# Performance work log

Measured on AMD Instinct MI355X. Metric: run time of the kernel, lower is better.

The kernel has to match this reference:

```python
import jax, jax.numpy as jnp
import numpy as np

B, D, C = 32768, 1024, 40  # batch, proj_dim, num_classes('culture')


def setup_inputs() -> dict:
    key = jax.random.key(0)
    k1, k2, k3, k4, k5 = jax.random.split(key, 5)
    scale = 1.0 / np.sqrt(D)
    return {
        "src": jax.random.normal(k1, (B, D), dtype=jnp.float32),
        "attn_mask": jnp.ones((B,), dtype=jnp.float32),  # unpacked but unused by BiChain
        # padded weights: row i uses only first D+i columns; the rest hit zero buffer slots
        "W": jax.random.normal(k2, (C, D + C), dtype=jnp.float32) * scale,
        "b": jax.random.normal(k3, (C,), dtype=jnp.float32) * scale,
        "W_rev": jax.random.normal(k4, (C, D + C), dtype=jnp.float32) * scale,
        "b_rev": jax.random.normal(k5, (C,), dtype=jnp.float32) * scale,
    }


def _chain(src, W, b):
    """Sequential classifier chain: score_i = sigmoid(<[src, s_0..s_{i-1}], w_i> + b_i)."""
    Bsz, Df = src.shape
    Cn = W.shape[0]
    # growing feature buffer, pre-padded with zeros for future scores
    buf0 = jnp.zeros((Bsz, Df + Cn), dtype=src.dtype).at[:, :Df].set(src)

    def step(buf, inp):
        w_i, b_i, i = inp
        score = jax.nn.sigmoid(buf @ w_i + b_i)            # [B]
        buf = jax.lax.dynamic_update_slice(buf, score[:, None], (0, Df + i))
        return buf, score

    _, scores = jax.lax.scan(step, buf0, (W, b, jnp.arange(Cn)))
    return scores.T  # [B, C]


def reference(src, attn_mask, W, b, W_rev, b_rev):
    out_fwd = _chain(src, W, b)
    out_rev = _chain(src, W_rev, b_rev)
    return (out_fwd + out_rev[:, ::-1]) * 0.5
```

## Files before the change

kernel.cpp:

```cpp
#include <hip/hip_runtime.h>
#include <math.h>

using short8  = __attribute__((ext_vector_type(8))) short;
using short4v = __attribute__((ext_vector_type(4))) short;
using float4v = __attribute__((ext_vector_type(4))) float;

#define D_DIM 1024
#define NCLS  40
#define WSTR  1064
#define TM    64
#define KC    64
#define NCHUNK 16
#define APAD  72

__device__ __forceinline__ short f2bf(float f) {
    union { float f; unsigned u; } x; x.f = f;
    unsigned r = (x.u + 0x7fffu + ((x.u >> 16) & 1u)) >> 16;
    return (short)r;
}

__global__ void convert_w_kernel(const float* __restrict__ W, const float* __restrict__ Wr,
                                 short* __restrict__ Wb) {
    int idx = blockIdx.x * 256 + threadIdx.x;
    int c = idx >> 10;
    int k = idx & 1023;
    float v = (c < NCLS) ? W[c * WSTR + k] : Wr[(c - NCLS) * WSTR + k];
    Wb[idx] = f2bf(v);
}

__global__ __launch_bounds__(256, 3) void bichain_main(
    const float* __restrict__ src, const short* __restrict__ Wb,
    const float* __restrict__ Wf, const float* __restrict__ Wr,
    const float* __restrict__ bf_, const float* __restrict__ br_,
    float* __restrict__ out)
{
    __shared__ __align__(16) unsigned char smem[41472];
    short* As = (short*)smem;
    short* Ws = (short*)(smem + 18432);

    const int tid  = threadIdx.x;
    const int lane = tid & 63;
    const int wave = tid >> 6;
    const int row0 = blockIdx.x * TM;

    const int s_row = tid >> 2;
    const int s_c4  = tid & 3;
    const float* srcRow = src + (long)(row0 + s_row) * D_DIM + s_c4 * 4;

    float4v a_reg[4];
    short8  w_reg[3];
    float4v acc[5];
#pragma unroll
    for (int t = 0; t < 5; ++t)
#pragma unroll
        for (int r = 0; r < 4; ++r) acc[t][r] = 0.f;

    auto load_regs = [&](int ch) {
        const int k0 = ch * KC;
#pragma unroll
        for (int j = 0; j < 4; ++j)
            a_reg[j] = *(const float4v*)(srcRow + k0 + j * 16);
#pragma unroll
        for (int r = 0; r < 3; ++r) {
            int idx = r * 256 + tid;
            if (r < 2 || tid < 128) {
                int cls = idx >> 3, oct = idx & 7;
                w_reg[r] = *(const short8*)(Wb + cls * D_DIM + k0 + oct * 8);
            }
        }
    };

    auto write_lds = [&](int buf) {
        short* Ab = As + buf * (TM * APAD);
#pragma unroll
        for (int j = 0; j < 4; ++j) {
            short4v v;
            v.x = f2bf(a_reg[j].x); v.y = f2bf(a_reg[j].y);
            v.z = f2bf(a_reg[j].z); v.w = f2bf(a_reg[j].w);
            *(short4v*)(Ab + s_row * APAD + j * 16 + s_c4 * 4) = v;
        }
        short* Wbuf = Ws + buf * (80 * APAD);
#pragma unroll
        for (int r = 0; r < 3; ++r) {
            int idx = r * 256 + tid;
            if (r < 2 || tid < 128) {
                int cls = idx >> 3, oct = idx & 7;
                *(short8*)(Wbuf + cls * APAD + oct * 8) = w_reg[r];
            }
        }
    };

    const int lrow = lane & 15;
    const int lk8  = (lane >> 4) * 8;

    auto compute = [&](int buf) {
        const short* Ab = As + buf * (TM * APAD) + (wave * 16) * APAD;
        const short* Wp = Ws + buf * (80 * APAD);
#pragma unroll
        for (int ks = 0; ks < 2; ++ks) {
            short8 af = *(const short8*)(Ab + lrow * APAD + ks * 32 + lk8);
#pragma unroll
            for (int t = 0; t < 5; ++t) {
                short8 bfr = *(const short8*)(Wp + (t * 16 + lrow) * APAD + ks * 32 + lk8);
                acc[t] = __builtin_amdgcn_mfma_f32_16x16x32_bf16(af, bfr, acc[t], 0, 0, 0);
            }
        }
    };

    load_regs(0);
    write_lds(0);
    __syncthreads();
#pragma unroll 1
    for (int ch = 0; ch < NCHUNK; ++ch) {
        const int cur = ch & 1;
        if (ch < NCHUNK - 1) load_regs(ch + 1);
        compute(cur);
        if (ch < NCHUNK - 1) {
            write_lds(cur ^ 1);
            __syncthreads();
        }
    }
    __syncthreads();

    float* Lg = (float*)smem;
    float* Sc = (float*)(smem + 20992);
#pragma unroll
    for (int t = 0; t < 5; ++t)
#pragma unroll
        for (int r = 0; r < 4; ++r) {
            int row = wave * 16 + (lane >> 4) * 4 + r;
            int cls = t * 16 + (lane & 15);
            Lg[row * 81 + cls] = acc[t][r];
        }
    __syncthreads();

    if (tid < 128) {
        const int row = tid >> 1;
        const int dir = tid & 1;
        const float* Wt = dir ? Wr : Wf;
        const float* bi = dir ? br_ : bf_;
        float s[NCLS];
#pragma unroll
        for (int i = 0; i < NCLS; ++i) {
            float z = Lg[row * 81 + dir * NCLS + i] + bi[i];
#pragma unroll
            for (int j = 0; j < i; ++j)
                z += s[j] * Wt[i * WSTR + D_DIM + j];
            s[i] = 1.f / (1.f + __expf(-z));
            Sc[row * 80 + dir * NCLS + i] = s[i];
        }
    }
    __syncthreads();

    float* outp = out + (long)row0 * NCLS;
    for (int idx = tid; idx < TM * NCLS; idx += 256) {
        int row = idx / NCLS;
        int c   = idx - row * NCLS;
        outp[idx] = 0.5f * (Sc[row * 80 + c] + Sc[row * 80 + NCLS + (NCLS - 1 - c)]);
    }
}

extern "C" void kernel_launch(void* const* d_in, const int* in_sizes, int n_in,
                              void* d_out, int out_size, void* d_ws, size_t ws_size,
                              hipStream_t stream) {
    const float* src = (const float*)d_in[0];
    const float* W   = (const float*)d_in[2];
    const float* b   = (const float*)d_in[3];
    const float* Wr  = (const float*)d_in[4];
    const float* br  = (const float*)d_in[5];
    float* out = (float*)d_out;
    short* Wb  = (short*)d_ws;

    convert_w_kernel<<<320, 256, 0, stream>>>(W, Wr, Wb);
    bichain_main<<<512, 256, 0, stream>>>(src, Wb, W, Wr, b, br, out);
}
```

Before: 42.15 us.

## Load MFMA operands directly from global memory, removing LDS staging and barriers

The GEMM main loop no longer stages A and W tiles through double-buffered LDS with a __syncthreads per chunk. Each lane now loads its src fragment straight from global memory, prefetched one chunk ahead, converts it to bf16 in registers, and reads W fragments directly from the bf16 weight buffer. This removes LDS write/read traffic and block barriers, at the cost of uncoalesced, strided global reads (each wave reads 16 rows and each lane reads W rows strided by D). The change also lowers the launch-bounds occupancy hint and switches to the library bf16 conversion.

```diff
diff --git a/kernel.cpp b/kernel.cpp
--- a/kernel.cpp
+++ b/kernel.cpp
@@ -1,22 +1,20 @@
 #include <hip/hip_runtime.h>
+#include <hip/hip_bf16.h>
 #include <math.h>
 
 using short8  = __attribute__((ext_vector_type(8))) short;
-using short4v = __attribute__((ext_vector_type(4))) short;
 using float4v = __attribute__((ext_vector_type(4))) float;
 
 #define D_DIM 1024
 #define NCLS  40
 #define WSTR  1064
 #define TM    64
-#define KC    64
 #define NCHUNK 16
-#define APAD  72
 
 __device__ __forceinline__ short f2bf(float f) {
-    union { float f; unsigned u; } x; x.f = f;
-    unsigned r = (x.u + 0x7fffu + ((x.u >> 16) & 1u)) >> 16;
-    return (short)r;
+    __hip_bfloat16 h = __float2bfloat16(f);
+    union { __hip_bfloat16 h; short s; } u; u.h = h;
+    return u.s;
 }
 
 __global__ void convert_w_kernel(const float* __restrict__ W, const float* __restrict__ Wr,
@@ -28,102 +26,65 @@
     Wb[idx] = f2bf(v);
 }
 
-__global__ __launch_bounds__(256, 3) void bichain_main(
+__global__ __launch_bounds__(256, 2) void bichain_main(
     const float* __restrict__ src, const short* __restrict__ Wb,
     const float* __restrict__ Wf, const float* __restrict__ Wr,
     const float* __restrict__ bf_, const float* __restrict__ br_,
     float* __restrict__ out)
 {
-    __shared__ __align__(16) unsigned char smem[41472];
-    short* As = (short*)smem;
-    short* Ws = (short*)(smem + 18432);
+    __shared__ float Lg[TM * 81];
+    __shared__ float Sc[TM * 80];
 
     const int tid  = threadIdx.x;
     const int lane = tid & 63;
     const int wave = tid >> 6;
     const int row0 = blockIdx.x * TM;
+    const int lrow = lane & 15;
+    const int lk8  = (lane >> 4) * 8;
 
-    const int s_row = tid >> 2;
-    const int s_c4  = tid & 3;
-    const float* srcRow = src + (long)(row0 + s_row) * D_DIM + s_c4 * 4;
+    const float* aRow = src + (size_t)(row0 + wave * 16 + lrow) * D_DIM + lk8;
+    const short* wRow = Wb + lrow * D_DIM + lk8;
 
-    float4v a_reg[4];
-    short8  w_reg[3];
     float4v acc[5];
 #pragma unroll
     for (int t = 0; t < 5; ++t)
 #pragma unroll
         for (int r = 0; r < 4; ++r) acc[t][r] = 0.f;
 
-    auto load_regs = [&](int ch) {
-        const int k0 = ch * KC;
+    float4v apre[4];
 #pragma unroll
-        for (int j = 0; j < 4; ++j)
-            a_reg[j] = *(const float4v*)(srcRow + k0 + j * 16);
+    for (int j = 0; j < 4; ++j)
+        apre[j] = *(const float4v*)(aRow + (j >> 1) * 32 + (j & 1) * 4);
+
+#pragma unroll 1
+    for (int ch = 0; ch < NCHUNK; ++ch) {
+        float4v a[4];
 #pragma unroll
-        for (int r = 0; r < 3; ++r) {
-            int idx = r * 256 + tid;
-            if (r < 2 || tid < 128) {
-                int cls = idx >> 3, oct = idx & 7;
-                w_reg[r] = *(const short8*)(Wb + cls * D_DIM + k0 + oct * 8);
+        for (int j = 0; j < 4; ++j) a[j] = apre[j];
+        if (ch < NCHUNK - 1) {
+            const float* nx = aRow + (ch + 1) * 64;
+#pragma unroll
+            for (int j = 0; j < 4; ++j)
+                apre[j] = *(const float4v*)(nx + (j >> 1) * 32 + (j & 1) * 4);
+        }
+        short8 af[2];
+#pragma unroll
+        for (int ks = 0; ks < 2; ++ks)
+#pragma unroll
+            for (int e = 0; e < 4; ++e) {
+                af[ks][e]     = f2bf(a[2 * ks][e]);
+                af[ks][e + 4] = f2bf(a[2 * ks + 1][e]);
             }
-        }
-    };
-
-    auto write_lds = [&](int buf) {
-        short* Ab = As + buf * (TM * APAD);
+        const short* wc = wRow + ch * 64;
 #pragma unroll
-        for (int j = 0; j < 4; ++j) {
-            short4v v;
-            v.x = f2bf(a_reg[j].x); v.y = f2bf(a_reg[j].y);
-            v.z = f2bf(a_reg[j].z); v.w = f2bf(a_reg[j].w);
-            *(short4v*)(Ab + s_row * APAD + j * 16 + s_c4 * 4) = v;
-        }
-        short* Wbuf = Ws + buf * (80 * APAD);
-#pragma unroll
-        for (int r = 0; r < 3; ++r) {
-            int idx = r * 256 + tid;
-            if (r < 2 || tid < 128) {
-                int cls = idx >> 3, oct = idx & 7;
-                *(short8*)(Wbuf + cls * APAD + oct * 8) = w_reg[r];
-            }
-        }
-    };
-
-    const int lrow = lane & 15;
-    const int lk8  = (lane >> 4) * 8;
-
-    auto compute = [&](int buf) {
-        const short* Ab = As + buf * (TM * APAD) + (wave * 16) * APAD;
-        const short* Wp = Ws + buf * (80 * APAD);
-#pragma unroll
-        for (int ks = 0; ks < 2; ++ks) {
-            short8 af = *(const short8*)(Ab + lrow * APAD + ks * 32 + lk8);
+        for (int ks = 0; ks < 2; ++ks)
 #pragma unroll
             for (int t = 0; t < 5; ++t) {
-                short8 bfr = *(const short8*)(Wp + (t * 16 + lrow) * APAD + ks * 32 + lk8);
-                acc[t] = __builtin_amdgcn_mfma_f32_16x16x32_bf16(af, bfr, acc[t], 0, 0, 0);
+                short8 bfr = *(const short8*)(wc + t * 16 * D_DIM + ks * 32);
+                acc[t] = __builtin_amdgcn_mfma_f32_16x16x32_bf16(af[ks], bfr, acc[t], 0, 0, 0);
             }
-        }
-    };
+    }
 
-    load_regs(0);
-    write_lds(0);
-    __syncthreads();
-#pragma unroll 1
-    for (int ch = 0; ch < NCHUNK; ++ch) {
-        const int cur = ch & 1;
-        if (ch < NCHUNK - 1) load_regs(ch + 1);
-        compute(cur);
-        if (ch < NCHUNK - 1) {
-            write_lds(cur ^ 1);
-            __syncthreads();
-        }
-    }
-    __syncthreads();
-
-    float* Lg = (float*)smem;
-    float* Sc = (float*)(smem + 20992);
 #pragma unroll
     for (int t = 0; t < 5; ++t)
 #pragma unroll
@@ -152,7 +113,7 @@
     }
     __syncthreads();
 
-    float* outp = out + (long)row0 * NCLS;
+    float* outp = out + (size_t)row0 * NCLS;
     for (int idx = tid; idx < TM * NCLS; idx += 256) {
         int row = idx / NCLS;
         int c   = idx - row * NCLS;
```

Result: slower. 73.94 us (+75.4%).
